# Kernel tuning notes

Measured on AMD Instinct MI355X. Metric: run time of the kernel, lower is better.

The kernel has to match this reference:

```python
import jax, jax.numpy as jnp
import numpy as np

K = 512
D = 128
BETA = 0.25
SOFTMIN_BETA = 10.0


def setup_inputs() -> dict:
    key = jax.random.key(0)
    k1, k2 = jax.random.split(key)
    latents = jax.random.normal(k1, (131072, D), dtype=jnp.float32)
    # embedding.weight.data.uniform_(-1/K, 1/K)
    emb_weight = jax.random.uniform(k2, (K, D), dtype=jnp.float32,
                                    minval=-1.0 / K, maxval=1.0 / K)
    return {"latents": latents, "emb_weight": emb_weight}


def reference(latents, emb_weight):
    # squared euclidean distances [B, K]
    dist = (jnp.sum(latents ** 2, axis=1, keepdims=True)
            + jnp.sum(emb_weight ** 2, axis=1)
            - 2.0 * jnp.matmul(latents, emb_weight.T))

    encoding_inds = jnp.argmin(dist, axis=1)                      # [B]
    # softmin(x) = softmax(-x)
    encoding_inds_soft = jax.nn.softmax(-SOFTMIN_BETA * dist, axis=1)  # [B, K]

    hard_one_hot = jax.nn.one_hot(encoding_inds, K, dtype=latents.dtype)
    # straight-through: hard in fwd, soft in bwd
    encoding_one_hot = (jax.lax.stop_gradient(hard_one_hot - encoding_inds_soft)
                        + encoding_inds_soft)

    quantized_latents = jnp.matmul(encoding_one_hot, emb_weight)  # [B, D]

    commitment_loss = jnp.mean((jax.lax.stop_gradient(quantized_latents) - latents) ** 2)
    embedding_loss = jnp.mean((quantized_latents - jax.lax.stop_gradient(latents)) ** 2)
    vq_loss = commitment_loss * BETA + embedding_loss

    avg_probs = jnp.mean(encoding_one_hot, axis=0)
    entropy_vq = -jnp.sum(avg_probs * jnp.log(avg_probs + 1e-10))

    # dist at the argmin position, averaged over batch
    cluster_metric = jnp.mean(jnp.take_along_axis(dist, encoding_inds[:, None], axis=1))

    return (quantized_latents, vq_loss, entropy_vq,
            encoding_inds[:, None], encoding_inds_soft, cluster_metric)
```

## Files before the change

kernel.cpp:

```cpp
#include <hip/hip_runtime.h>

using u32 = unsigned int;

constexpr int B = 131072;
constexpr int K = 512;
constexpr int D = 128;
constexpr int RPB = 64;
constexpr int RG  = 8;
constexpr int NG  = RPB / RG;
constexpr float SMBETA = 10.0f;

constexpr size_t OFF_Q    = 0;
constexpr size_t OFF_VQ   = (size_t)B * D;
constexpr size_t OFF_ENT  = OFF_VQ + 1;
constexpr size_t OFF_INDS = OFF_VQ + 2;
constexpr size_t OFF_SOFT = OFF_INDS + (size_t)B;
constexpr size_t OFF_CL   = OFF_SOFT + (size_t)B * K;

__global__ __launch_bounds__(512) void vq_main(
    const float* __restrict__ X, const float* __restrict__ E,
    float* __restrict__ out,
    u32* __restrict__ counts,
    float* __restrict__ sse_g, float* __restrict__ clus_g)
{
  __shared__ float gbuf[RG][K];
  __shared__ float sx_sh[RG];
  __shared__ float m_sh[RG];
  __shared__ int   amin_sh[RG];
  __shared__ float invS_sh[RG];
  __shared__ float red_sh[16];

  const int tid  = threadIdx.x;
  const int j    = tid;
  const int w    = tid >> 6;
  const int lane = tid & 63;
  const int row0 = blockIdx.x * RPB;

  const float4* Ej4 = (const float4*)(E + (size_t)j * D);
  float4 ereg[32];
  #pragma unroll
  for (int s = 0; s < 32; ++s) ereg[s] = Ej4[s];

  double seD = 0.0;
  #pragma unroll
  for (int s = 0; s < 32; ++s) {
    float e0 = ereg[s].x; seD += (double)(e0 * e0);
    float e1 = ereg[s].y; seD += (double)(e1 * e1);
    float e2 = ereg[s].z; seD += (double)(e2 * e2);
    float e3 = ereg[s].w; seD += (double)(e3 * e3);
  }
  const float se = (float)seD;

  float sse_l = 0.f, msum_l = 0.f;

  #pragma unroll 1
  for (int gi = 0; gi < NG; ++gi) {
    const int grow0 = row0 + gi * RG;

    {
      const float* xr = X + (size_t)(grow0 + w) * D;
      float v0 = xr[lane], v1 = xr[lane + 64];
      float s0 = v0 * v0, s1 = v1 * v1;
      double t = (double)s0 + (double)s1;
      for (int mk = 1; mk < 64; mk <<= 1) t += __shfl_xor(t, mk, 64);
      if (lane == 0) sx_sh[w] = (float)t;
    }
    __syncthreads();

    const float4* xg4 = (const float4*)(X + (size_t)grow0 * D);
    float acc[RG];
    #pragma unroll
    for (int r = 0; r < RG; ++r) acc[r] = 0.f;

    #pragma unroll
    for (int s = 0; s < 32; ++s) {
      float4 e4 = ereg[s];
      #pragma unroll
      for (int r = 0; r < RG; ++r) {
        float4 x4 = xg4[r * 32 + s];
        float a = acc[r];
        a = fmaf(e4.x, x4.x, a);
        a = fmaf(e4.y, x4.y, a);
        a = fmaf(e4.z, x4.z, a);
        a = fmaf(e4.w, x4.w, a);
        acc[r] = a;
      }
    }

    float dq[RG];
    #pragma unroll
    for (int r = 0; r < RG; ++r) {
      float a = sx_sh[r] + se;
      dq[r] = a - 2.0f * acc[r];
      gbuf[r][j] = dq[r];
    }
    __syncthreads();

    {
      float mv = 3.4e38f; int mi = 0;
      #pragma unroll
      for (int k2 = 0; k2 < 8; ++k2) {
        int jj = lane + 64 * k2;
        float v = gbuf[w][jj];
        if (v < mv || (v == mv && jj < mi)) { mv = v; mi = jj; }
      }
      for (int mk = 1; mk < 64; mk <<= 1) {
        float ov = __shfl_xor(mv, mk, 64);
        int   oi = __shfl_xor(mi, mk, 64);
        if (ov < mv || (ov == mv && oi < mi)) { mv = ov; mi = oi; }
      }
      if (lane == 0) { m_sh[w] = mv; amin_sh[w] = mi; }
    }
    __syncthreads();

    float p[RG];
    #pragma unroll
    for (int r = 0; r < RG; ++r) {
      p[r] = __expf(-SMBETA * (dq[r] - m_sh[r]));
      gbuf[r][j] = p[r];
    }
    __syncthreads();

    {
      float sv = 0.f;
      #pragma unroll
      for (int k2 = 0; k2 < 8; ++k2) sv += gbuf[w][lane + 64 * k2];
      for (int mk = 1; mk < 64; mk <<= 1) sv += __shfl_xor(sv, mk, 64);
      if (lane == 0) invS_sh[w] = 1.f / sv;
    }
    __syncthreads();

    #pragma unroll
    for (int r = 0; r < RG; ++r) {
      size_t row = (size_t)(grow0 + r);
      out[OFF_SOFT + row * K + j] = p[r] * invS_sh[r];
    }

    {
      int row = grow0 + w;
      int am  = amin_sh[w];
      const float* xr = X + (size_t)row * D;
      const float* er = E + (size_t)am * D;
      #pragma unroll
      for (int t = 0; t < 2; ++t) {
        int d = lane + 64 * t;
        float xv = xr[d], ev = er[d];
        float df = ev - xv;
        sse_l = fmaf(df, df, sse_l);
        out[OFF_Q + (size_t)row * D + d] = ev;
      }
      if (lane == 0) {
        out[OFF_INDS + row] = (float)am;
        atomicAdd(&counts[am], 1u);
        msum_l += m_sh[w];
      }
    }
    __syncthreads();
  }

  for (int mk = 1; mk < 64; mk <<= 1) {
    sse_l  += __shfl_xor(sse_l,  mk, 64);
    msum_l += __shfl_xor(msum_l, mk, 64);
  }
  if (lane == 0) { red_sh[w] = sse_l; red_sh[8 + w] = msum_l; }
  __syncthreads();
  if (tid == 0) {
    float s1 = 0.f, s2 = 0.f;
    for (int q = 0; q < 8; ++q) { s1 += red_sh[q]; s2 += red_sh[8 + q]; }
    atomicAdd(sse_g, s1);
    atomicAdd(clus_g, s2);
  }
}

__global__ __launch_bounds__(512) void vq_final(
    const u32* __restrict__ counts,
    const float* __restrict__ sse_g, const float* __restrict__ clus_g,
    float* __restrict__ out)
{
  __shared__ double part[8];
  const int tid = threadIdx.x, w = tid >> 6, lane = tid & 63;
  double pv = (double)counts[tid] / (double)B;
  double term = -pv * log(pv + 1e-10);
  for (int mk = 1; mk < 64; mk <<= 1) term += __shfl_xor(term, mk, 64);
  if (lane == 0) part[w] = term;
  __syncthreads();
  if (tid == 0) {
    double ent = 0.0;
    for (int q = 0; q < 8; ++q) ent += part[q];
    double sse = (double)*sse_g;
    double vq  = 1.25 * sse / ((double)B * (double)D);
    double cl  = (double)*clus_g / (double)B;
    out[OFF_VQ]  = (float)vq;
    out[OFF_ENT] = (float)ent;
    out[OFF_CL]  = (float)cl;
  }
}

extern "C" void kernel_launch(void* const* d_in, const int* in_sizes, int n_in,
                              void* d_out, int out_size, void* d_ws, size_t ws_size,
                              hipStream_t stream) {
  const float* X = (const float*)d_in[0];
  const float* E = (const float*)d_in[1];
  if (n_in >= 2 && in_sizes[0] == K * D && in_sizes[1] == B * D) {
    const float* t = X; X = E; E = t;
  }
  float* out = (float*)d_out;

  u32*   counts = (u32*)d_ws;
  float* sse_g  = (float*)((char*)d_ws + 2048);
  float* clus_g = (float*)((char*)d_ws + 2052);

  hipMemsetAsync(d_ws, 0, 4096, stream);
  vq_main<<<B / RPB, 512, 0, stream>>>(X, E, out, counts, sse_g, clus_g);
  vq_final<<<1, 512, 0, stream>>>(counts, sse_g, clus_g, out);
}
```

Baseline: 903.7 us.

## Compute all 64 row distances at once with chunked codebook loads instead of register-resident codebook

The per-thread codebook row is no longer held in 32 float4 registers. It is streamed in chunks of four float4s, and each thread accumulates dot products for all 64 rows of the block in a 64-entry accumulator array. The row norms are precomputed for all 64 rows before the matmul, and the later per-group softmax loop is fully unrolled to index into the accumulator array. The swap changes register pressure (from 128 codebook floats to 64 accumulators) and amortises each codebook load over more rows. It risks spills or lower occupancy from fully unrolling the post-processing loop and indexing acc by gi.

Measured after the change: 1.480 ms. 63.8% more time.

```diff
diff --git a/kernel.cpp b/kernel.cpp
--- a/kernel.cpp
+++ b/kernel.cpp
@@ -8,6 +8,8 @@
 constexpr int RPB = 64;
 constexpr int RG  = 8;
 constexpr int NG  = RPB / RG;
+constexpr int CH  = 4;
+constexpr int NCH = (D / 4) / CH;
 constexpr float SMBETA = 10.0f;
 
 constexpr size_t OFF_Q    = 0;
@@ -24,7 +26,7 @@
     float* __restrict__ sse_g, float* __restrict__ clus_g)
 {
   __shared__ float gbuf[RG][K];
-  __shared__ float sx_sh[RG];
+  __shared__ float sx_sh[RPB];
   __shared__ float m_sh[RG];
   __shared__ int   amin_sh[RG];
   __shared__ float invS_sh[RG];
@@ -36,64 +38,71 @@
   const int lane = tid & 63;
   const int row0 = blockIdx.x * RPB;
 
+  #pragma unroll 1
+  for (int t = 0; t < NG; ++t) {
+    const int rr = t * RG + w;
+    const float* xr = X + (size_t)(row0 + rr) * D;
+    float v0 = xr[lane], v1 = xr[lane + 64];
+    float s0 = v0 * v0, s1 = v1 * v1;
+    double tt = (double)s0 + (double)s1;
+    for (int mk = 1; mk < 64; mk <<= 1) tt += __shfl_xor(tt, mk, 64);
+    if (lane == 0) sx_sh[rr] = (float)tt;
+  }
+  __syncthreads();
+
+  const float4* xg4 = (const float4*)(X + (size_t)row0 * D);
   const float4* Ej4 = (const float4*)(E + (size_t)j * D);
-  float4 ereg[32];
+
+  float acc[RPB];
   #pragma unroll
-  for (int s = 0; s < 32; ++s) ereg[s] = Ej4[s];
+  for (int r = 0; r < RPB; ++r) acc[r] = 0.f;
 
   double seD = 0.0;
+
+  #pragma unroll 1
+  for (int c = 0; c < NCH; ++c) {
+    float4 e4[CH];
+    #pragma unroll
+    for (int s = 0; s < CH; ++s) e4[s] = Ej4[c * CH + s];
+
+    #pragma unroll
+    for (int s = 0; s < CH; ++s) {
+      float e0 = e4[s].x; seD += (double)(e0 * e0);
+      float e1 = e4[s].y; seD += (double)(e1 * e1);
+      float e2 = e4[s].z; seD += (double)(e2 * e2);
+      float e3 = e4[s].w; seD += (double)(e3 * e3);
+    }
+
+    #pragma unroll
+    for (int s = 0; s < CH; ++s) {
+      #pragma unroll
+      for (int r = 0; r < RPB; ++r) {
+        float4 x4 = xg4[r * 32 + c * CH + s];
+        float a = acc[r];
+        a = fmaf(e4[s].x, x4.x, a);
+        a = fmaf(e4[s].y, x4.y, a);
+        a = fmaf(e4[s].z, x4.z, a);
+        a = fmaf(e4[s].w, x4.w, a);
+        acc[r] = a;
+      }
+    }
+  }
+  const float se = (float)seD;
+
   #pragma unroll
-  for (int s = 0; s < 32; ++s) {
-    float e0 = ereg[s].x; seD += (double)(e0 * e0);
-    float e1 = ereg[s].y; seD += (double)(e1 * e1);
-    float e2 = ereg[s].z; seD += (double)(e2 * e2);
-    float e3 = ereg[s].w; seD += (double)(e3 * e3);
-  }
-  const float se = (float)seD;
+  for (int r = 0; r < RPB; ++r) {
+    float a = sx_sh[r] + se;
+    acc[r] = a - 2.0f * acc[r];
+  }
 
   float sse_l = 0.f, msum_l = 0.f;
 
-  #pragma unroll 1
+  #pragma unroll
   for (int gi = 0; gi < NG; ++gi) {
     const int grow0 = row0 + gi * RG;
 
-    {
-      const float* xr = X + (size_t)(grow0 + w) * D;
-      float v0 = xr[lane], v1 = xr[lane + 64];
-      float s0 = v0 * v0, s1 = v1 * v1;
-      double t = (double)s0 + (double)s1;
-      for (int mk = 1; mk < 64; mk <<= 1) t += __shfl_xor(t, mk, 64);
-      if (lane == 0) sx_sh[w] = (float)t;
-    }
-    __syncthreads();
-
-    const float4* xg4 = (const float4*)(X + (size_t)grow0 * D);
-    float acc[RG];
-    #pragma unroll
-    for (int r = 0; r < RG; ++r) acc[r] = 0.f;
-
-    #pragma unroll
-    for (int s = 0; s < 32; ++s) {
-      float4 e4 = ereg[s];
-      #pragma unroll
-      for (int r = 0; r < RG; ++r) {
-        float4 x4 = xg4[r * 32 + s];
-        float a = acc[r];
-        a = fmaf(e4.x, x4.x, a);
-        a = fmaf(e4.y, x4.y, a);
-        a = fmaf(e4.z, x4.z, a);
-        a = fmaf(e4.w, x4.w, a);
-        acc[r] = a;
-      }
-    }
-
-    float dq[RG];
-    #pragma unroll
-    for (int r = 0; r < RG; ++r) {
-      float a = sx_sh[r] + se;
-      dq[r] = a - 2.0f * acc[r];
-      gbuf[r][j] = dq[r];
-    }
+    #pragma unroll
+    for (int r = 0; r < RG; ++r) gbuf[r][j] = acc[gi * RG + r];
     __syncthreads();
 
     {
@@ -116,7 +125,7 @@
     float p[RG];
     #pragma unroll
     for (int r = 0; r < RG; ++r) {
-      p[r] = __expf(-SMBETA * (dq[r] - m_sh[r]));
+      p[r] = __expf(-SMBETA * (acc[gi * RG + r] - m_sh[r]));
       gbuf[r][j] = p[r];
     }
     __syncthreads();
```
